# Optimization experiments

Measured on AMD Instinct MI355X. Metric: run time of the kernel, lower is better.

The kernel has to match this reference:

```python
import jax, jax.numpy as jnp
import numpy as np

LAMBDA_C = 10.0
LAMBDA_E = 10.0
LAMBDA_O = 10.0
H = 0.1          # proximity / thickness scale from __init__ h=0.1
EPS = 1e-8


def _pairwise_sq(a, b):
    # a [N,3], b [M,3] -> [N,M] squared distances
    return jnp.sum((a[:, None, :] - b[None, :, :]) ** 2, axis=-1)


def _total_loss(pred_vertices, face_probs, target_vertices, pred_faces, target_faces):
    pv, tv, probs = pred_vertices, target_vertices, face_probs

    # ---- chamfer loss (bidirectional mean of NN squared distances) ----
    d2_pt = _pairwise_sq(pv, tv)                       # [N, M]
    chamfer = d2_pt.min(axis=1).mean() + d2_pt.min(axis=0).mean()

    # ---- probabilistic surface distance via face barycenters ----
    tri = pv[pred_faces]                               # [F,3,3]
    ttri = tv[target_faces]                            # [Ft,3,3]
    bp = tri.mean(axis=1)                              # [F,3]
    bt = ttri.mean(axis=1)                             # [Ft,3]
    d2_f = _pairwise_sq(bp, bt)                        # [F,Ft]
    surface = (probs * d2_f.min(axis=1)).mean() + d2_f.min(axis=0).mean()

    # ---- shared pairwise geometry ----
    v0, v1, v2 = tri[:, 0], tri[:, 1], tri[:, 2]
    n = jnp.cross(v1 - v0, v2 - v0)                    # [F,3] face normals
    nhat = n / (jnp.linalg.norm(n, axis=-1, keepdims=True) + EPS)
    F_ = tri.shape[0]
    mask = 1.0 - jnp.eye(F_, dtype=pv.dtype)           # exclude self pairs
    cd2 = _pairwise_sq(bp, bp)                         # [F,F] centroid dist^2
    gate = jnp.exp(-cd2 / H)                           # soft spatial proximity gate

    # ---- triangle collision: vertices of tri j vs plane of tri i ----
    # s[i,j,v] = nhat_i . (tri[j,v] - v0_i)
    s = jnp.einsum('id,fvd->ifv', nhat, tri) - jnp.einsum('id,id->i', nhat, v0)[:, None, None]
    pen_col = jax.nn.relu(-(s.max(-1) * s.min(-1)))    # >0 iff tri j straddles plane i
    collision = (probs[:, None] * mask * gate * pen_col).sum() / F_

    # ---- edge crossing: segment-segment closest distance, all 9 edge pairs ----
    p = tri                                            # edge starts [F,3,3]
    q = jnp.roll(tri, -1, axis=1)                      # edge ends   [F,3,3]
    p1 = p[:, None, :, None, :]                        # [F,1,3,1,3]
    q1 = q[:, None, :, None, :]
    p2 = p[None, :, None, :, :]                        # [1,F,1,3,3]
    q2 = q[None, :, None, :, :]
    d1 = q1 - p1
    d2 = q2 - p2
    r = p1 - p2
    a = jnp.sum(d1 * d1, -1)
    e = jnp.sum(d2 * d2, -1)
    f = jnp.sum(d2 * r, -1)
    c = jnp.sum(d1 * r, -1)
    b = jnp.sum(d1 * d2, -1)
    denom = a * e - b * b
    sseg = jnp.clip((b * f - c * e) / (denom + EPS), 0.0, 1.0)
    tseg = jnp.clip((b * sseg + f) / (e + EPS), 0.0, 1.0)
    sseg = jnp.clip((b * tseg - c) / (a + EPS), 0.0, 1.0)
    cp1 = p1 + sseg[..., None] * d1
    cp2 = p2 + tseg[..., None] * d2
    dist = jnp.sqrt(jnp.sum((cp1 - cp2) ** 2, -1) + EPS)   # [F,F,3,3]
    pen_edge = jax.nn.relu(H - dist).sum((-1, -2))          # [F,F]
    edge_crossing = (probs[:, None] * mask * gate * pen_edge).sum() / F_

    # ---- triangle overlap: centroid of tri j close to plane of tri i ----
    dp = jnp.abs(jnp.einsum('id,jd->ij', nhat, bp) - jnp.einsum('id,id->i', nhat, v0)[:, None])
    pen_ov = jax.nn.relu(H - dp)                            # [F,F]
    overlap = (probs[:, None] * mask * gate * pen_ov).sum() / F_

    return (chamfer + surface
            + LAMBDA_C * collision
            + LAMBDA_E * edge_crossing
            + LAMBDA_O * overlap)


def setup_inputs() -> dict:
    key = jax.random.key(0)
    k1, k2, k3, k4, k5 = jax.random.split(key, 5)
    N, F, M, Ft = 512, 1024, 32768, 65536
    return {
        'pred_vertices': jax.random.normal(k1, (N, 3), dtype=jnp.float32),
        'face_probs': jax.random.uniform(k2, (F,), dtype=jnp.float32),
        'target_vertices': jax.random.normal(k3, (M, 3), dtype=jnp.float32),
        'pred_faces': jax.random.randint(k4, (F, 3), 0, N),
        'target_faces': jax.random.randint(k5, (Ft, 3), 0, M),
    }


def reference(pred_vertices, face_probs, target_vertices, pred_faces, target_faces):
    return _total_loss(pred_vertices, face_probs, target_vertices, pred_faces, target_faces)
```

## Files before the change

kernel.cpp:

```cpp
#include <hip/hip_runtime.h>
#include <hip/hip_bf16.h>
#include <math.h>

#define EPSF 1e-8f
#define HPARAM 0.1f
#define FB 16
#define NC 16
#define VB 8
#define NCM 16

__device__ __forceinline__ float waveReduceSum(float v) {
#pragma unroll
    for (int o = 32; o > 0; o >>= 1) v += __shfl_down(v, o, 64);
    return v;
}
__device__ __forceinline__ float waveReduceMin(float v) {
#pragma unroll
    for (int o = 32; o > 0; o >>= 1) v = fminf(v, __shfl_down(v, o, 64));
    return v;
}
__device__ __forceinline__ float blockSum(float s, float* red4) {
    s = waveReduceSum(s);
    int lane = threadIdx.x & 63, wid = threadIdx.x >> 6;
    if (lane == 0) red4[wid] = s;
    __syncthreads();
    return red4[0] + red4[1] + red4[2] + red4[3];
}
__device__ __forceinline__ float clamp01(float x) {
    return fminf(fmaxf(x, 0.0f), 1.0f);
}

__global__ __launch_bounds__(256) void k_pre(
    const float* __restrict__ pv, const int* __restrict__ pf,
    const float* __restrict__ tv, const int* __restrict__ tf,
    float* __restrict__ tri, float4* __restrict__ bp4,
    float* __restrict__ nhat, float* __restrict__ d0,
    float4* __restrict__ bt4, float4* __restrict__ tv4, float4* __restrict__ pv4,
    int N, int F, int M, int Ft)
{
    int nbF = (F + 255) >> 8, nbFt = (Ft + 255) >> 8, nbM = (M + 255) >> 8;
    int b = blockIdx.x, tid = threadIdx.x;
    if (b < nbF) {
        int i = b * 256 + tid;
        if (i >= F) return;
        int a = pf[i * 3 + 0], bb = pf[i * 3 + 1], c = pf[i * 3 + 2];
        float v0x = pv[a * 3], v0y = pv[a * 3 + 1], v0z = pv[a * 3 + 2];
        float v1x = pv[bb * 3], v1y = pv[bb * 3 + 1], v1z = pv[bb * 3 + 2];
        float v2x = pv[c * 3], v2y = pv[c * 3 + 1], v2z = pv[c * 3 + 2];
        tri[i * 9 + 0] = v0x; tri[i * 9 + 1] = v0y; tri[i * 9 + 2] = v0z;
        tri[i * 9 + 3] = v1x; tri[i * 9 + 4] = v1y; tri[i * 9 + 5] = v1z;
        tri[i * 9 + 6] = v2x; tri[i * 9 + 7] = v2y; tri[i * 9 + 8] = v2z;
        float bx = (v0x + v1x + v2x) / 3.0f;
        float by = (v0y + v1y + v2y) / 3.0f;
        float bz = (v0z + v1z + v2z) / 3.0f;
        bp4[i] = make_float4(bx, by, bz, bx * bx + by * by + bz * bz);
        float e1x = v1x - v0x, e1y = v1y - v0y, e1z = v1z - v0z;
        float e2x = v2x - v0x, e2y = v2y - v0y, e2z = v2z - v0z;
        float nx = e1y * e2z - e1z * e2y;
        float ny = e1z * e2x - e1x * e2z;
        float nz = e1x * e2y - e1y * e2x;
        float nrm = sqrtf(nx * nx + ny * ny + nz * nz);
        float inv = 1.0f / (nrm + EPSF);
        float hx = nx * inv, hy = ny * inv, hz = nz * inv;
        nhat[i * 3 + 0] = hx; nhat[i * 3 + 1] = hy; nhat[i * 3 + 2] = hz;
        d0[i] = hx * v0x + hy * v0y + hz * v0z;
    } else if (b < nbF + nbFt) {
        int j = (b - nbF) * 256 + tid;
        if (j >= Ft) return;
        int a = tf[j * 3 + 0], bb = tf[j * 3 + 1], c = tf[j * 3 + 2];
        float bx = (tv[a * 3 + 0] + tv[bb * 3 + 0] + tv[c * 3 + 0]) / 3.0f;
        float by = (tv[a * 3 + 1] + tv[bb * 3 + 1] + tv[c * 3 + 1]) / 3.0f;
        float bz = (tv[a * 3 + 2] + tv[bb * 3 + 2] + tv[c * 3 + 2]) / 3.0f;
        bt4[j] = make_float4(bx, by, bz, bx * bx + by * by + bz * bz);
    } else if (b < nbF + nbFt + nbM) {
        int j = (b - nbF - nbFt) * 256 + tid;
        if (j >= M) return;
        float x = tv[j * 3], y = tv[j * 3 + 1], z = tv[j * 3 + 2];
        tv4[j] = make_float4(x, y, z, x * x + y * y + z * z);
    } else {
        int j = (b - nbF - nbFt - nbM) * 256 + tid;
        if (j >= N) return;
        float x = pv[j * 3], y = pv[j * 3 + 1], z = pv[j * 3 + 2];
        pv4[j] = make_float4(x, y, z, x * x + y * y + z * z);
    }
}

__global__ __launch_bounds__(256) void k_mega(
    const float4* __restrict__ pv4, const float4* __restrict__ tv4,
    const float* __restrict__ tri, const float4* __restrict__ bp4,
    const float* __restrict__ nhat, const float* __restrict__ d0,
    const float* __restrict__ probs, const float4* __restrict__ bt4,
    float* __restrict__ chamAp, float* __restrict__ chamBp,
    float* __restrict__ surfAp, float* __restrict__ surfBp,
    float* __restrict__ pairp,
    int N, int F, int M, int Ft, int ncS, int ncC,
    int o1, int o2, int o3, int o4)
{
    __shared__ float4 sh4[1024];
    __shared__ float red4[4];
    int b = blockIdx.x;
    int tid = threadIdx.x;

    if (b < o1) {
        int fg = b & 63, chunk = b >> 6;
        int i0 = fg * FB;
        float m2x[FB], m2y[FB], m2z[FB], psq[FB], m[FB];
#pragma unroll
        for (int k = 0; k < FB; ++k) {
            float4 bb = bp4[i0 + k];
            m2x[k] = -2.0f * bb.x; m2y[k] = -2.0f * bb.y; m2z[k] = -2.0f * bb.z;
            psq[k] = bb.w;
            m[k] = 3.4e38f;
        }
        int TC = Ft / NC;
        int jend = chunk * TC + TC;
        for (int j = chunk * TC + tid; j < jend; j += 256) {
            float4 t = bt4[j];
#pragma unroll
            for (int k = 0; k < FB; ++k) {
                float acc = fmaf(m2x[k], t.x, fmaf(m2y[k], t.y, fmaf(m2z[k], t.z, psq[k] + t.w)));
                m[k] = fminf(m[k], acc);
            }
        }
        __shared__ float redA[4][FB];
#pragma unroll
        for (int k = 0; k < FB; ++k) m[k] = waveReduceMin(m[k]);
        int lane = tid & 63, wid = tid >> 6;
        if (lane == 0) {
#pragma unroll
            for (int k = 0; k < FB; ++k) redA[wid][k] = m[k];
        }
        __syncthreads();
        if (tid < FB) {
            float r = fminf(fminf(redA[0][tid], redA[1][tid]),
                            fminf(redA[2][tid], redA[3][tid]));
            surfAp[(i0 + tid) * NC + chunk] = r;
        }
    } else if (b < o2) {
        int rb = b - o1;
        int jg = rb & 63, c = rb >> 6;
        int CH = F / ncS;
        for (int t = tid; t < CH; t += 256) {
            float4 p = bp4[c * CH + t];
            sh4[t] = make_float4(-2.0f * p.x, -2.0f * p.y, -2.0f * p.z, p.w);
        }
        __syncthreads();
        int q = Ft >> 2;
        int j0 = jg * 256 + tid;
        float4 t0 = bt4[j0], t1 = bt4[j0 + q], t2 = bt4[j0 + 2 * q], t3 = bt4[j0 + 3 * q];
        float m0 = 3.4e38f, m1 = 3.4e38f, m2 = 3.4e38f, m3 = 3.4e38f;
#pragma unroll 4
        for (int i = 0; i < CH; ++i) {
            float4 p = sh4[i];
            m0 = fminf(m0, fmaf(p.x, t0.x, fmaf(p.y, t0.y, fmaf(p.z, t0.z, p.w + t0.w))));
            m1 = fminf(m1, fmaf(p.x, t1.x, fmaf(p.y, t1.y, fmaf(p.z, t1.z, p.w + t1.w))));
            m2 = fminf(m2, fmaf(p.x, t2.x, fmaf(p.y, t2.y, fmaf(p.z, t2.z, p.w + t2.w))));
            m3 = fminf(m3, fmaf(p.x, t3.x, fmaf(p.y, t3.y, fmaf(p.z, t3.z, p.w + t3.w))));
        }
        surfBp[c * Ft + j0] = m0;
        surfBp[c * Ft + j0 + q] = m1;
        surfBp[c * Ft + j0 + 2 * q] = m2;
        surfBp[c * Ft + j0 + 3 * q] = m3;
    } else if (b < o3) {
        int rb = b - o2;
        int vg = rb & 63, chunk = rb >> 6;
        int v0 = vg * VB;
        float m2x[VB], m2y[VB], m2z[VB], psq[VB], m[VB];
#pragma unroll
        for (int k = 0; k < VB; ++k) {
            float4 p = pv4[v0 + k];
            m2x[k] = -2.0f * p.x; m2y[k] = -2.0f * p.y; m2z[k] = -2.0f * p.z;
            psq[k] = p.w;
            m[k] = 3.4e38f;
        }
        int TC = M / NCM;
        int jend = chunk * TC + TC;
        for (int j = chunk * TC + tid; j < jend; j += 256) {
            float4 t = tv4[j];
#pragma unroll
            for (int k = 0; k < VB; ++k) {
                float acc = fmaf(m2x[k], t.x, fmaf(m2y[k], t.y, fmaf(m2z[k], t.z, psq[k] + t.w)));
                m[k] = fminf(m[k], acc);
            }
        }
        __shared__ float redC[4][VB];
#pragma unroll
        for (int k = 0; k < VB; ++k) m[k] = waveReduceMin(m[k]);
        int lane = tid & 63, wid = tid >> 6;
        if (lane == 0) {
#pragma unroll
            for (int k = 0; k < VB; ++k) redC[wid][k] = m[k];
        }
        __syncthreads();
        if (tid < VB) {
            float r = fminf(fminf(redC[0][tid], redC[1][tid]),
                            fminf(redC[2][tid], redC[3][tid]));
            chamAp[(v0 + tid) * NCM + chunk] = r;
        }
    } else if (b < o4) {
        int rb = b - o3;
        int jg = rb & 31, c = rb >> 5;
        int CH = N / ncC;
        for (int t = tid; t < CH; t += 256) {
            float4 p = pv4[c * CH + t];
            sh4[t] = make_float4(-2.0f * p.x, -2.0f * p.y, -2.0f * p.z, p.w);
        }
        __syncthreads();
        int q = M >> 2;
        int j0 = jg * 256 + tid;
        float4 t0 = tv4[j0], t1 = tv4[j0 + q], t2 = tv4[j0 + 2 * q], t3 = tv4[j0 + 3 * q];
        float m0 = 3.4e38f, m1 = 3.4e38f, m2 = 3.4e38f, m3 = 3.4e38f;
#pragma unroll 4
        for (int i = 0; i < CH; ++i) {
            float4 p = sh4[i];
            m0 = fminf(m0, fmaf(p.x, t0.x, fmaf(p.y, t0.y, fmaf(p.z, t0.z, p.w + t0.w))));
            m1 = fminf(m1, fmaf(p.x, t1.x, fmaf(p.y, t1.y, fmaf(p.z, t1.z, p.w + t1.w))));
            m2 = fminf(m2, fmaf(p.x, t2.x, fmaf(p.y, t2.y, fmaf(p.z, t2.z, p.w + t2.w))));
            m3 = fminf(m3, fmaf(p.x, t3.x, fmaf(p.y, t3.y, fmaf(p.z, t3.z, p.w + t3.w))));
        }
        chamBp[c * M + j0] = m0;
        chamBp[c * M + j0 + q] = m1;
        chamBp[c * M + j0 + 2 * q] = m2;
        chamBp[c * M + j0 + 3 * q] = m3;
    } else {
        int rb = b - o4;
        int bpF = F >> 8;
        int i = rb / bpF;
        int fg = rb % bpF;
        float* sTri = (float*)sh4;
        for (int t = tid; t < 256 * 9; t += 256) sTri[t] = tri[fg * 256 * 9 + t];
        __syncthreads();
        int f = fg * 256 + tid;

        float ti[9];
#pragma unroll
        for (int v = 0; v < 9; ++v) ti[v] = tri[i * 9 + v];
        float nix = nhat[i * 3], niy = nhat[i * 3 + 1], niz = nhat[i * 3 + 2];
        float di = d0[i];
        float4 bi = bp4[i];
        float pi = probs[i];

        float p1xa[3], p1ya[3], p1za[3], d1xa[3], d1ya[3], d1za[3], ava[3], rava[3];
#pragma unroll
        for (int e1 = 0; e1 < 3; ++e1) {
            int e1n = (e1 == 2) ? 0 : e1 + 1;
            p1xa[e1] = ti[e1 * 3]; p1ya[e1] = ti[e1 * 3 + 1]; p1za[e1] = ti[e1 * 3 + 2];
            d1xa[e1] = ti[e1n * 3] - p1xa[e1];
            d1ya[e1] = ti[e1n * 3 + 1] - p1ya[e1];
            d1za[e1] = ti[e1n * 3 + 2] - p1za[e1];
            ava[e1] = d1xa[e1] * d1xa[e1] + d1ya[e1] * d1ya[e1] + d1za[e1] * d1za[e1];
            rava[e1] = __builtin_amdgcn_rcpf(ava[e1] + EPSF);
        }

        float contrib = 0.0f;
        if (f != i) {
            float4 bf = bp4[f];
            float cdx = bi.x - bf.x, cdy = bi.y - bf.y, cdz = bi.z - bf.z;
            float cd2 = cdx * cdx + cdy * cdy + cdz * cdz;
            if (cd2 <= 2.0f) {
                float gate = __expf(-10.0f * cd2);
                float tf9[9];
#pragma unroll
                for (int v = 0; v < 9; ++v) tf9[v] = sTri[tid * 9 + v];
                float s0 = nix * tf9[0] + niy * tf9[1] + niz * tf9[2] - di;
                float s1 = nix * tf9[3] + niy * tf9[4] + niz * tf9[5] - di;
                float s2 = nix * tf9[6] + niy * tf9[7] + niz * tf9[8] - di;
                float smax = fmaxf(fmaxf(s0, s1), s2);
                float smin = fminf(fminf(s0, s1), s2);
                float pen_col = fmaxf(-(smax * smin), 0.0f);
                float dp = fabsf(nix * bf.x + niy * bf.y + niz * bf.z - di);
                float pen_ov = fmaxf(HPARAM - dp, 0.0f);
                float q2x[3], q2y[3], q2z[3], e2xa[3], e2ya[3], e2za[3], eva[3], reva[3];
#pragma unroll
                for (int e2 = 0; e2 < 3; ++e2) {
                    int e2n = (e2 == 2) ? 0 : e2 + 1;
                    q2x[e2] = tf9[e2 * 3]; q2y[e2] = tf9[e2 * 3 + 1]; q2z[e2] = tf9[e2 * 3 + 2];
                    e2xa[e2] = tf9[e2n * 3] - q2x[e2];
                    e2ya[e2] = tf9[e2n * 3 + 1] - q2y[e2];
                    e2za[e2] = tf9[e2n * 3 + 2] - q2z[e2];
                    eva[e2] = e2xa[e2] * e2xa[e2] + e2ya[e2] * e2ya[e2] + e2za[e2] * e2za[e2];
                    reva[e2] = __builtin_amdgcn_rcpf(eva[e2] + EPSF);
                }
                float pen_edge = 0.0f;
#pragma unroll
                for (int e1 = 0; e1 < 3; ++e1) {
#pragma unroll
                    for (int e2 = 0; e2 < 3; ++e2) {
                        float rx = p1xa[e1] - q2x[e2], ry = p1ya[e1] - q2y[e2], rz = p1za[e1] - q2z[e2];
                        float f_ = e2xa[e2] * rx + e2ya[e2] * ry + e2za[e2] * rz;
                        float c_ = d1xa[e1] * rx + d1ya[e1] * ry + d1za[e1] * rz;
                        float b_ = d1xa[e1] * e2xa[e2] + d1ya[e1] * e2ya[e2] + d1za[e1] * e2za[e2];
                        float denom = ava[e1] * eva[e2] - b_ * b_;
                        float rden = __builtin_amdgcn_rcpf(denom + EPSF);
                        float ss = clamp01(fmaf(-c_, eva[e2], b_ * f_) * rden);
                        float tt = clamp01(fmaf(b_, ss, f_) * reva[e2]);
                        ss = clamp01(fmaf(b_, tt, -c_) * rava[e1]);
                        float vx = fmaf(ss, d1xa[e1], p1xa[e1]) - fmaf(tt, e2xa[e2], q2x[e2]);
                        float vy = fmaf(ss, d1ya[e1], p1ya[e1]) - fmaf(tt, e2ya[e2], q2y[e2]);
                        float vz = fmaf(ss, d1za[e1], p1za[e1]) - fmaf(tt, e2za[e2], q2z[e2]);
                        float dist = __builtin_amdgcn_sqrtf(vx * vx + vy * vy + vz * vz + EPSF);
                        pen_edge += fmaxf(HPARAM - dist, 0.0f);
                    }
                }
                contrib = pi * gate * (pen_col + pen_ov + pen_edge);
            }
        }
        float s = blockSum(contrib, red4);
        if (tid == 0) pairp[rb] = s;
    }
}

__global__ __launch_bounds__(256) void k_reduce(
    const float* __restrict__ surfBp, int Ft, int ncS, float invFt,
    const float* __restrict__ chamBp, int M, int ncC, float invM,
    const float* __restrict__ chamAp, int N, float invN,
    const float* __restrict__ surfAp, const float* __restrict__ probs, int F, float invF,
    const float* __restrict__ pairp, float pairScale,
    float* __restrict__ smallp)
{
    __shared__ float red4[4];
    int b = blockIdx.x, tid = threadIdx.x;
    int nbS = Ft >> 8, nbC = M >> 8, nbA = N >> 8, nbSA = F >> 8;
    float s;
    if (b < nbS) {
        int j = b * 256 + tid;
        float r = 3.4e38f;
        for (int c = 0; c < ncS; ++c) r = fminf(r, surfBp[c * Ft + j]);
        s = r * invFt;
    } else if (b < nbS + nbC) {
        int j = (b - nbS) * 256 + tid;
        float r = 3.4e38f;
        for (int c = 0; c < ncC; ++c) r = fminf(r, chamBp[c * M + j]);
        s = r * invM;
    } else if (b < nbS + nbC + nbA) {
        int v = (b - nbS - nbC) * 256 + tid;
        float r = 3.4e38f;
#pragma unroll
        for (int c = 0; c < NCM; ++c) r = fminf(r, chamAp[v * NCM + c]);
        s = r * invN;
    } else if (b < nbS + nbC + nbA + nbSA) {
        int i = (b - nbS - nbC - nbA) * 256 + tid;
        float r = 3.4e38f;
#pragma unroll
        for (int c = 0; c < NC; ++c) r = fminf(r, surfAp[i * NC + c]);
        s = probs[i] * r * invF;
    } else {
        int t = (b - nbS - nbC - nbA - nbSA) * 256 + tid;
        s = pairp[t] * pairScale;
    }
    float r = blockSum(s, red4);
    if (tid == 0) smallp[b] = r;
}

__global__ __launch_bounds__(256) void k_fin(
    const float* __restrict__ smallp, int n, float* __restrict__ out)
{
    __shared__ float red4[4];
    float s = 0.0f;
    for (int t = threadIdx.x; t < n; t += 256) s += smallp[t];
    float r = blockSum(s, red4);
    if (threadIdx.x == 0) out[0] = r;
}

extern "C" void kernel_launch(void* const* d_in, const int* in_sizes, int n_in,
                              void* d_out, int out_size, void* d_ws, size_t ws_size,
                              hipStream_t stream) {
    const float* pv    = (const float*)d_in[0];
    const float* probs = (const float*)d_in[1];
    const float* tv    = (const float*)d_in[2];
    const int*   pf    = (const int*)d_in[3];
    const int*   tf    = (const int*)d_in[4];
    float* out = (float*)d_out;

    int N  = in_sizes[0] / 3;
    int F  = in_sizes[1];
    int M  = in_sizes[2] / 3;
    int Ft = in_sizes[4] / 3;

    int nP = F * (F / 256);

    size_t baseFloats = (size_t)F * 13 + (size_t)F * 4 + (size_t)Ft * 4
                      + (size_t)M * 4 + (size_t)N * 4
                      + (size_t)N * NCM + (size_t)F * NC + (size_t)nP + 512;
    int ncS = 8, ncC = 8;
    if (ws_size < (baseFloats + (size_t)8 * Ft + (size_t)8 * M) * 4) {
        ncS = 2; ncC = 2;
        if (ws_size < (baseFloats + (size_t)2 * Ft + (size_t)2 * M) * 4) { ncS = 1; ncC = 1; }
    }

    float* ws = (float*)d_ws;
    float* w_tri    = ws;
    float* w_nhat   = w_tri + F * 9;
    float* w_d0     = w_nhat + F * 3;
    float4* w_bp4   = (float4*)(w_d0 + F);
    float4* w_bt4   = w_bp4 + F;
    float4* w_tv4   = w_bt4 + Ft;
    float4* w_pv4   = w_tv4 + M;
    float* w_chamAp = (float*)(w_pv4 + N);
    float* w_surfAp = w_chamAp + N * NCM;
    float* w_pair   = w_surfAp + F * NC;
    float* w_small  = w_pair + nP;
    float* w_surfBp = w_small + 512;
    float* w_chamBp = w_surfBp + (size_t)ncS * Ft;

    int gSurfA = (F / FB) * NC;
    int gSurfB = (Ft / 4 / 256) * ncS;
    int gChamA = (N / VB) * NCM;
    int gChamB = (M / 4 / 256) * ncC;
    int o1 = gSurfA;
    int o2 = o1 + gSurfB;
    int o3 = o2 + gChamA;
    int o4 = o3 + gChamB;
    int gTot = o4 + nP;

    int nSmall = (Ft >> 8) + (M >> 8) + (N >> 8) + (F >> 8) + (nP >> 8);
    int gPre = (F + 255) / 256 + (Ft + 255) / 256 + (M + 255) / 256 + (N + 255) / 256;

    k_pre<<<gPre, 256, 0, stream>>>(
        pv, pf, tv, tf, w_tri, w_bp4, w_nhat, w_d0, w_bt4, w_tv4, w_pv4, N, F, M, Ft);
    k_mega<<<gTot, 256, 0, stream>>>(
        w_pv4, w_tv4, w_tri, w_bp4, w_nhat, w_d0, probs, w_bt4,
        w_chamAp, w_chamBp, w_surfAp, w_surfBp, w_pair,
        N, F, M, Ft, ncS, ncC, o1, o2, o3, o4);
    k_reduce<<<nSmall, 256, 0, stream>>>(
        w_surfBp, Ft, ncS, 1.0f / (float)Ft,
        w_chamBp, M, ncC, 1.0f / (float)M,
        w_chamAp, N, 1.0f / (float)N,
        w_surfAp, probs, F, 1.0f / (float)F,
        w_pair, 10.0f / (float)F,
        w_small);
    k_fin<<<1, 256, 0, stream>>>(w_small, nSmall, out);
}
```

Measured before the change: 50.60 us.

## Fuse column-min passes into row-min loops and compact pair candidates

The separate column-direction nearest-neighbour passes for surface and chamfer are removed. Instead, the row-min loops also write a per-group column minimum for each target point, which k_reduce then folds across groups. This reuses the distance evaluations already computed instead of recomputing the full distance matrix twice. It costs far more partial writes (64 groups per target for both surface and chamfer) and a heavier reduction pass. The pair kernel also compacts proximity-passing candidates with ballot and prefix sums to cut divergence, and skips the nine square roots when the minimum edge distance exceeds H.

```diff
diff --git a/kernel.cpp b/kernel.cpp
--- a/kernel.cpp
+++ b/kernel.cpp
@@ -93,10 +93,9 @@
     float* __restrict__ chamAp, float* __restrict__ chamBp,
     float* __restrict__ surfAp, float* __restrict__ surfBp,
     float* __restrict__ pairp,
-    int N, int F, int M, int Ft, int ncS, int ncC,
-    int o1, int o2, int o3, int o4)
+    int N, int F, int M, int Ft,
+    int o1, int o2)
 {
-    __shared__ float4 sh4[1024];
     __shared__ float red4[4];
     int b = blockIdx.x;
     int tid = threadIdx.x;
@@ -116,11 +115,14 @@
         int jend = chunk * TC + TC;
         for (int j = chunk * TC + tid; j < jend; j += 256) {
             float4 t = bt4[j];
+            float jm = 3.4e38f;
 #pragma unroll
             for (int k = 0; k < FB; ++k) {
                 float acc = fmaf(m2x[k], t.x, fmaf(m2y[k], t.y, fmaf(m2z[k], t.z, psq[k] + t.w)));
                 m[k] = fminf(m[k], acc);
-            }
+                jm = fminf(jm, acc);
+            }
+            surfBp[fg * Ft + j] = jm;
         }
         __shared__ float redA[4][FB];
 #pragma unroll
@@ -138,31 +140,6 @@
         }
     } else if (b < o2) {
         int rb = b - o1;
-        int jg = rb & 63, c = rb >> 6;
-        int CH = F / ncS;
-        for (int t = tid; t < CH; t += 256) {
-            float4 p = bp4[c * CH + t];
-            sh4[t] = make_float4(-2.0f * p.x, -2.0f * p.y, -2.0f * p.z, p.w);
-        }
-        __syncthreads();
-        int q = Ft >> 2;
-        int j0 = jg * 256 + tid;
-        float4 t0 = bt4[j0], t1 = bt4[j0 + q], t2 = bt4[j0 + 2 * q], t3 = bt4[j0 + 3 * q];
-        float m0 = 3.4e38f, m1 = 3.4e38f, m2 = 3.4e38f, m3 = 3.4e38f;
-#pragma unroll 4
-        for (int i = 0; i < CH; ++i) {
-            float4 p = sh4[i];
-            m0 = fminf(m0, fmaf(p.x, t0.x, fmaf(p.y, t0.y, fmaf(p.z, t0.z, p.w + t0.w))));
-            m1 = fminf(m1, fmaf(p.x, t1.x, fmaf(p.y, t1.y, fmaf(p.z, t1.z, p.w + t1.w))));
-            m2 = fminf(m2, fmaf(p.x, t2.x, fmaf(p.y, t2.y, fmaf(p.z, t2.z, p.w + t2.w))));
-            m3 = fminf(m3, fmaf(p.x, t3.x, fmaf(p.y, t3.y, fmaf(p.z, t3.z, p.w + t3.w))));
-        }
-        surfBp[c * Ft + j0] = m0;
-        surfBp[c * Ft + j0 + q] = m1;
-        surfBp[c * Ft + j0 + 2 * q] = m2;
-        surfBp[c * Ft + j0 + 3 * q] = m3;
-    } else if (b < o3) {
-        int rb = b - o2;
         int vg = rb & 63, chunk = rb >> 6;
         int v0 = vg * VB;
         float m2x[VB], m2y[VB], m2z[VB], psq[VB], m[VB];
@@ -177,11 +154,14 @@
         int jend = chunk * TC + TC;
         for (int j = chunk * TC + tid; j < jend; j += 256) {
             float4 t = tv4[j];
+            float jm = 3.4e38f;
 #pragma unroll
             for (int k = 0; k < VB; ++k) {
                 float acc = fmaf(m2x[k], t.x, fmaf(m2y[k], t.y, fmaf(m2z[k], t.z, psq[k] + t.w)));
                 m[k] = fminf(m[k], acc);
-            }
+                jm = fminf(jm, acc);
+            }
+            chamBp[vg * M + j] = jm;
         }
         __shared__ float redC[4][VB];
 #pragma unroll
@@ -197,40 +177,16 @@
                             fminf(redC[2][tid], redC[3][tid]));
             chamAp[(v0 + tid) * NCM + chunk] = r;
         }
-    } else if (b < o4) {
-        int rb = b - o3;
-        int jg = rb & 31, c = rb >> 5;
-        int CH = N / ncC;
-        for (int t = tid; t < CH; t += 256) {
-            float4 p = pv4[c * CH + t];
-            sh4[t] = make_float4(-2.0f * p.x, -2.0f * p.y, -2.0f * p.z, p.w);
-        }
-        __syncthreads();
-        int q = M >> 2;
-        int j0 = jg * 256 + tid;
-        float4 t0 = tv4[j0], t1 = tv4[j0 + q], t2 = tv4[j0 + 2 * q], t3 = tv4[j0 + 3 * q];
-        float m0 = 3.4e38f, m1 = 3.4e38f, m2 = 3.4e38f, m3 = 3.4e38f;
-#pragma unroll 4
-        for (int i = 0; i < CH; ++i) {
-            float4 p = sh4[i];
-            m0 = fminf(m0, fmaf(p.x, t0.x, fmaf(p.y, t0.y, fmaf(p.z, t0.z, p.w + t0.w))));
-            m1 = fminf(m1, fmaf(p.x, t1.x, fmaf(p.y, t1.y, fmaf(p.z, t1.z, p.w + t1.w))));
-            m2 = fminf(m2, fmaf(p.x, t2.x, fmaf(p.y, t2.y, fmaf(p.z, t2.z, p.w + t2.w))));
-            m3 = fminf(m3, fmaf(p.x, t3.x, fmaf(p.y, t3.y, fmaf(p.z, t3.z, p.w + t3.w))));
-        }
-        chamBp[c * M + j0] = m0;
-        chamBp[c * M + j0 + q] = m1;
-        chamBp[c * M + j0 + 2 * q] = m2;
-        chamBp[c * M + j0 + 3 * q] = m3;
     } else {
-        int rb = b - o4;
+        __shared__ float sTri[256 * 9];
+        __shared__ int slist[256];
+        __shared__ float scd2[256];
+        __shared__ int scnt[4];
+        int rb = b - o2;
         int bpF = F >> 8;
         int i = rb / bpF;
         int fg = rb % bpF;
-        float* sTri = (float*)sh4;
         for (int t = tid; t < 256 * 9; t += 256) sTri[t] = tri[fg * 256 * 9 + t];
-        __syncthreads();
-        int f = fg * 256 + tid;
 
         float ti[9];
 #pragma unroll
@@ -252,58 +208,81 @@
             rava[e1] = __builtin_amdgcn_rcpf(ava[e1] + EPSF);
         }
 
+        int f = fg * 256 + tid;
+        float4 bft = bp4[f];
+        float cdx = bi.x - bft.x, cdy = bi.y - bft.y, cdz = bi.z - bft.z;
+        float cd2 = cdx * cdx + cdy * cdy + cdz * cdz;
+        bool pass = (f != i) && (cd2 <= 2.0f);
+        unsigned long long mask = __ballot(pass);
+        int lane = tid & 63, wid = tid >> 6;
+        if (lane == 0) scnt[wid] = __popcll(mask);
+        __syncthreads();
+        int base = 0;
+#pragma unroll
+        for (int w = 0; w < 4; ++w) base += (w < wid) ? scnt[w] : 0;
+        int nCand = scnt[0] + scnt[1] + scnt[2] + scnt[3];
+        int pfx = __popcll(mask & ((1ULL << lane) - 1ULL));
+        if (pass) { slist[base + pfx] = tid; scd2[base + pfx] = cd2; }
+        __syncthreads();
+
         float contrib = 0.0f;
-        if (f != i) {
-            float4 bf = bp4[f];
-            float cdx = bi.x - bf.x, cdy = bi.y - bf.y, cdz = bi.z - bf.z;
-            float cd2 = cdx * cdx + cdy * cdy + cdz * cdz;
-            if (cd2 <= 2.0f) {
-                float gate = __expf(-10.0f * cd2);
-                float tf9[9];
-#pragma unroll
-                for (int v = 0; v < 9; ++v) tf9[v] = sTri[tid * 9 + v];
-                float s0 = nix * tf9[0] + niy * tf9[1] + niz * tf9[2] - di;
-                float s1 = nix * tf9[3] + niy * tf9[4] + niz * tf9[5] - di;
-                float s2 = nix * tf9[6] + niy * tf9[7] + niz * tf9[8] - di;
-                float smax = fmaxf(fmaxf(s0, s1), s2);
-                float smin = fminf(fminf(s0, s1), s2);
-                float pen_col = fmaxf(-(smax * smin), 0.0f);
-                float dp = fabsf(nix * bf.x + niy * bf.y + niz * bf.z - di);
-                float pen_ov = fmaxf(HPARAM - dp, 0.0f);
-                float q2x[3], q2y[3], q2z[3], e2xa[3], e2ya[3], e2za[3], eva[3], reva[3];
+        if (tid < nCand) {
+            int src = slist[tid];
+            float cc = scd2[tid];
+            float gate = __expf(-10.0f * cc);
+            float4 bf = bp4[fg * 256 + src];
+            float tf9[9];
+#pragma unroll
+            for (int v = 0; v < 9; ++v) tf9[v] = sTri[src * 9 + v];
+            float s0 = nix * tf9[0] + niy * tf9[1] + niz * tf9[2] - di;
+            float s1 = nix * tf9[3] + niy * tf9[4] + niz * tf9[5] - di;
+            float s2 = nix * tf9[6] + niy * tf9[7] + niz * tf9[8] - di;
+            float smax = fmaxf(fmaxf(s0, s1), s2);
+            float smin = fminf(fminf(s0, s1), s2);
+            float pen_col = fmaxf(-(smax * smin), 0.0f);
+            float dp = fabsf(nix * bf.x + niy * bf.y + niz * bf.z - di);
+            float pen_ov = fmaxf(HPARAM - dp, 0.0f);
+            float q2x[3], q2y[3], q2z[3], e2xa[3], e2ya[3], e2za[3], eva[3], reva[3];
+#pragma unroll
+            for (int e2 = 0; e2 < 3; ++e2) {
+                int e2n = (e2 == 2) ? 0 : e2 + 1;
+                q2x[e2] = tf9[e2 * 3]; q2y[e2] = tf9[e2 * 3 + 1]; q2z[e2] = tf9[e2 * 3 + 2];
+                e2xa[e2] = tf9[e2n * 3] - q2x[e2];
+                e2ya[e2] = tf9[e2n * 3 + 1] - q2y[e2];
+                e2za[e2] = tf9[e2n * 3 + 2] - q2z[e2];
+                eva[e2] = e2xa[e2] * e2xa[e2] + e2ya[e2] * e2ya[e2] + e2za[e2] * e2za[e2];
+                reva[e2] = __builtin_amdgcn_rcpf(eva[e2] + EPSF);
+            }
+            float d2v[9];
+            float dminv = 3.4e38f;
+#pragma unroll
+            for (int e1 = 0; e1 < 3; ++e1) {
 #pragma unroll
                 for (int e2 = 0; e2 < 3; ++e2) {
-                    int e2n = (e2 == 2) ? 0 : e2 + 1;
-                    q2x[e2] = tf9[e2 * 3]; q2y[e2] = tf9[e2 * 3 + 1]; q2z[e2] = tf9[e2 * 3 + 2];
-                    e2xa[e2] = tf9[e2n * 3] - q2x[e2];
-                    e2ya[e2] = tf9[e2n * 3 + 1] - q2y[e2];
-                    e2za[e2] = tf9[e2n * 3 + 2] - q2z[e2];
-                    eva[e2] = e2xa[e2] * e2xa[e2] + e2ya[e2] * e2ya[e2] + e2za[e2] * e2za[e2];
-                    reva[e2] = __builtin_amdgcn_rcpf(eva[e2] + EPSF);
+                    float rx = p1xa[e1] - q2x[e2], ry = p1ya[e1] - q2y[e2], rz = p1za[e1] - q2z[e2];
+                    float f_ = e2xa[e2] * rx + e2ya[e2] * ry + e2za[e2] * rz;
+                    float c_ = d1xa[e1] * rx + d1ya[e1] * ry + d1za[e1] * rz;
+                    float b_ = d1xa[e1] * e2xa[e2] + d1ya[e1] * e2ya[e2] + d1za[e1] * e2za[e2];
+                    float denom = ava[e1] * eva[e2] - b_ * b_;
+                    float rden = __builtin_amdgcn_rcpf(denom + EPSF);
+                    float ss = clamp01(fmaf(-c_, eva[e2], b_ * f_) * rden);
+                    float tt = clamp01(fmaf(b_, ss, f_) * reva[e2]);
+                    ss = clamp01(fmaf(b_, tt, -c_) * rava[e1]);
+                    float vx = fmaf(ss, d1xa[e1], p1xa[e1]) - fmaf(tt, e2xa[e2], q2x[e2]);
+                    float vy = fmaf(ss, d1ya[e1], p1ya[e1]) - fmaf(tt, e2ya[e2], q2y[e2]);
+                    float vz = fmaf(ss, d1za[e1], p1za[e1]) - fmaf(tt, e2za[e2], q2z[e2]);
+                    float dd = vx * vx + vy * vy + vz * vz;
+                    d2v[e1 * 3 + e2] = dd;
+                    dminv = fminf(dminv, dd);
                 }
-                float pen_edge = 0.0f;
-#pragma unroll
-                for (int e1 = 0; e1 < 3; ++e1) {
-#pragma unroll
-                    for (int e2 = 0; e2 < 3; ++e2) {
-                        float rx = p1xa[e1] - q2x[e2], ry = p1ya[e1] - q2y[e2], rz = p1za[e1] - q2z[e2];
-                        float f_ = e2xa[e2] * rx + e2ya[e2] * ry + e2za[e2] * rz;
-                        float c_ = d1xa[e1] * rx + d1ya[e1] * ry + d1za[e1] * rz;
-                        float b_ = d1xa[e1] * e2xa[e2] + d1ya[e1] * e2ya[e2] + d1za[e1] * e2za[e2];
-                        float denom = ava[e1] * eva[e2] - b_ * b_;
-                        float rden = __builtin_amdgcn_rcpf(denom + EPSF);
-                        float ss = clamp01(fmaf(-c_, eva[e2], b_ * f_) * rden);
-                        float tt = clamp01(fmaf(b_, ss, f_) * reva[e2]);
-                        ss = clamp01(fmaf(b_, tt, -c_) * rava[e1]);
-                        float vx = fmaf(ss, d1xa[e1], p1xa[e1]) - fmaf(tt, e2xa[e2], q2x[e2]);
-                        float vy = fmaf(ss, d1ya[e1], p1ya[e1]) - fmaf(tt, e2ya[e2], q2y[e2]);
-                        float vz = fmaf(ss, d1za[e1], p1za[e1]) - fmaf(tt, e2za[e2], q2z[e2]);
-                        float dist = __builtin_amdgcn_sqrtf(vx * vx + vy * vy + vz * vz + EPSF);
-                        pen_edge += fmaxf(HPARAM - dist, 0.0f);
-                    }
-                }
-                contrib = pi * gate * (pen_col + pen_ov + pen_edge);
-            }
+            }
+            float pen_edge = 0.0f;
+            if (dminv + EPSF < HPARAM * HPARAM) {
+#pragma unroll
+                for (int q = 0; q < 9; ++q)
+                    pen_edge += fmaxf(HPARAM - __builtin_amdgcn_sqrtf(d2v[q] + EPSF), 0.0f);
+            }
+            contrib = pi * gate * (pen_col + pen_ov + pen_edge);
         }
         float s = blockSum(contrib, red4);
         if (tid == 0) pairp[rb] = s;
@@ -311,8 +290,8 @@
 }
 
 __global__ __launch_bounds__(256) void k_reduce(
-    const float* __restrict__ surfBp, int Ft, int ncS, float invFt,
-    const float* __restrict__ chamBp, int M, int ncC, float invM,
+    const float* __restrict__ surfBp, int Ft, int nGS, float invFt,
+    const float* __restrict__ chamBp, int M, int nGC, float invM,
     const float* __restrict__ chamAp, int N, float invN,
     const float* __restrict__ surfAp, const float* __restrict__ probs, int F, float invF,
     const float* __restrict__ pairp, float pairScale,
@@ -325,12 +304,12 @@
     if (b < nbS) {
         int j = b * 256 + tid;
         float r = 3.4e38f;
-        for (int c = 0; c < ncS; ++c) r = fminf(r, surfBp[c * Ft + j]);
+        for (int c = 0; c < nGS; ++c) r = fminf(r, surfBp[c * Ft + j]);
         s = r * invFt;
     } else if (b < nbS + nbC) {
         int j = (b - nbS) * 256 + tid;
         float r = 3.4e38f;
-        for (int c = 0; c < ncC; ++c) r = fminf(r, chamBp[c * M + j]);
+        for (int c = 0; c < nGC; ++c) r = fminf(r, chamBp[c * M + j]);
         s = r * invM;
     } else if (b < nbS + nbC + nbA) {
         int v = (b - nbS - nbC) * 256 + tid;
@@ -377,16 +356,9 @@
     int M  = in_sizes[2] / 3;
     int Ft = in_sizes[4] / 3;
 
-    int nP = F * (F / 256);
-
-    size_t baseFloats = (size_t)F * 13 + (size_t)F * 4 + (size_t)Ft * 4
-                      + (size_t)M * 4 + (size_t)N * 4
-                      + (size_t)N * NCM + (size_t)F * NC + (size_t)nP + 512;
-    int ncS = 8, ncC = 8;
-    if (ws_size < (baseFloats + (size_t)8 * Ft + (size_t)8 * M) * 4) {
-        ncS = 2; ncC = 2;
-        if (ws_size < (baseFloats + (size_t)2 * Ft + (size_t)2 * M) * 4) { ncS = 1; ncC = 1; }
-    }
+    int nP  = F * (F / 256);
+    int nGS = F / FB;
+    int nGC = N / VB;
 
     float* ws = (float*)d_ws;
     float* w_tri    = ws;
@@ -401,17 +373,11 @@
     float* w_pair   = w_surfAp + F * NC;
     float* w_small  = w_pair + nP;
     float* w_surfBp = w_small + 512;
-    float* w_chamBp = w_surfBp + (size_t)ncS * Ft;
-
-    int gSurfA = (F / FB) * NC;
-    int gSurfB = (Ft / 4 / 256) * ncS;
-    int gChamA = (N / VB) * NCM;
-    int gChamB = (M / 4 / 256) * ncC;
-    int o1 = gSurfA;
-    int o2 = o1 + gSurfB;
-    int o3 = o2 + gChamA;
-    int o4 = o3 + gChamB;
-    int gTot = o4 + nP;
+    float* w_chamBp = w_surfBp + (size_t)nGS * Ft;
+
+    int o1 = (F / FB) * NC;
+    int o2 = o1 + (N / VB) * NCM;
+    int gTot = o2 + nP;
 
     int nSmall = (Ft >> 8) + (M >> 8) + (N >> 8) + (F >> 8) + (nP >> 8);
     int gPre = (F + 255) / 256 + (Ft + 255) / 256 + (M + 255) / 256 + (N + 255) / 256;
@@ -421,10 +387,10 @@
     k_mega<<<gTot, 256, 0, stream>>>(
         w_pv4, w_tv4, w_tri, w_bp4, w_nhat, w_d0, probs, w_bt4,
         w_chamAp, w_chamBp, w_surfAp, w_surfBp, w_pair,
-        N, F, M, Ft, ncS, ncC, o1, o2, o3, o4);
+        N, F, M, Ft, o1, o2);
     k_reduce<<<nSmall, 256, 0, stream>>>(
-        w_surfBp, Ft, ncS, 1.0f / (float)Ft,
-        w_chamBp, M, ncC, 1.0f / (float)M,
+        w_surfBp, Ft, nGS, 1.0f / (float)Ft,
+        w_chamBp, M, nGC, 1.0f / (float)M,
         w_chamAp, N, 1.0f / (float)N,
         w_surfAp, probs, F, 1.0f / (float)F,
         w_pair, 10.0f / (float)F,
```

Result: slower. 65.63 us (+29.7%).

## Compact gated pair candidates per block, hoist norm terms, fuse final reduce

Applied to the files above, without the earlier changes.

The pairwise penalty section now handles several faces per block. It compacts the candidate pairs that pass the proximity gate into a shared list using ballot and prefix counts, so the active lanes run the heavy segment math densely instead of diverging. The per-pair edge sqrt work is skipped unless the minimum squared distance is inside the threshold. The squared-norm terms in the nearest-neighbour min loops are moved out of the inner loop and added after the min. The final single-block kernel is replaced by a last-block-done atomic counter inside the reduce kernel, which adds extra __syncthreads per face iteration and a counter reset.

```diff
diff --git a/kernel.cpp b/kernel.cpp
--- a/kernel.cpp
+++ b/kernel.cpp
@@ -8,6 +8,7 @@
 #define NC 16
 #define VB 8
 #define NCM 16
+#define TI 4
 
 __device__ __forceinline__ float waveReduceSum(float v) {
 #pragma unroll
@@ -36,8 +37,10 @@
     float* __restrict__ tri, float4* __restrict__ bp4,
     float* __restrict__ nhat, float* __restrict__ d0,
     float4* __restrict__ bt4, float4* __restrict__ tv4, float4* __restrict__ pv4,
+    int* __restrict__ cnt,
     int N, int F, int M, int Ft)
 {
+    if (blockIdx.x == 0 && threadIdx.x == 0) *cnt = 0;
     int nbF = (F + 255) >> 8, nbFt = (Ft + 255) >> 8, nbM = (M + 255) >> 8;
     int b = blockIdx.x, tid = threadIdx.x;
     if (b < nbF) {
@@ -94,7 +97,7 @@
     float* __restrict__ surfAp, float* __restrict__ surfBp,
     float* __restrict__ pairp,
     int N, int F, int M, int Ft, int ncS, int ncC,
-    int o1, int o2, int o3, int o4)
+    int o1, int o2, int o3)
 {
     __shared__ float4 sh4[1024];
     __shared__ float red4[4];
@@ -104,12 +107,11 @@
     if (b < o1) {
         int fg = b & 63, chunk = b >> 6;
         int i0 = fg * FB;
-        float m2x[FB], m2y[FB], m2z[FB], psq[FB], m[FB];
+        float m2x[FB], m2y[FB], m2z[FB], m[FB];
 #pragma unroll
         for (int k = 0; k < FB; ++k) {
             float4 bb = bp4[i0 + k];
             m2x[k] = -2.0f * bb.x; m2y[k] = -2.0f * bb.y; m2z[k] = -2.0f * bb.z;
-            psq[k] = bb.w;
             m[k] = 3.4e38f;
         }
         int TC = Ft / NC;
@@ -118,7 +120,7 @@
             float4 t = bt4[j];
 #pragma unroll
             for (int k = 0; k < FB; ++k) {
-                float acc = fmaf(m2x[k], t.x, fmaf(m2y[k], t.y, fmaf(m2z[k], t.z, psq[k] + t.w)));
+                float acc = fmaf(m2x[k], t.x, fmaf(m2y[k], t.y, fmaf(m2z[k], t.z, t.w)));
                 m[k] = fminf(m[k], acc);
             }
         }
@@ -134,7 +136,7 @@
         if (tid < FB) {
             float r = fminf(fminf(redA[0][tid], redA[1][tid]),
                             fminf(redA[2][tid], redA[3][tid]));
-            surfAp[(i0 + tid) * NC + chunk] = r;
+            surfAp[(i0 + tid) * NC + chunk] = r + bp4[i0 + tid].w;
         }
     } else if (b < o2) {
         int rb = b - o1;
@@ -152,25 +154,24 @@
 #pragma unroll 4
         for (int i = 0; i < CH; ++i) {
             float4 p = sh4[i];
-            m0 = fminf(m0, fmaf(p.x, t0.x, fmaf(p.y, t0.y, fmaf(p.z, t0.z, p.w + t0.w))));
-            m1 = fminf(m1, fmaf(p.x, t1.x, fmaf(p.y, t1.y, fmaf(p.z, t1.z, p.w + t1.w))));
-            m2 = fminf(m2, fmaf(p.x, t2.x, fmaf(p.y, t2.y, fmaf(p.z, t2.z, p.w + t2.w))));
-            m3 = fminf(m3, fmaf(p.x, t3.x, fmaf(p.y, t3.y, fmaf(p.z, t3.z, p.w + t3.w))));
-        }
-        surfBp[c * Ft + j0] = m0;
-        surfBp[c * Ft + j0 + q] = m1;
-        surfBp[c * Ft + j0 + 2 * q] = m2;
-        surfBp[c * Ft + j0 + 3 * q] = m3;
+            m0 = fminf(m0, fmaf(p.x, t0.x, fmaf(p.y, t0.y, fmaf(p.z, t0.z, p.w))));
+            m1 = fminf(m1, fmaf(p.x, t1.x, fmaf(p.y, t1.y, fmaf(p.z, t1.z, p.w))));
+            m2 = fminf(m2, fmaf(p.x, t2.x, fmaf(p.y, t2.y, fmaf(p.z, t2.z, p.w))));
+            m3 = fminf(m3, fmaf(p.x, t3.x, fmaf(p.y, t3.y, fmaf(p.z, t3.z, p.w))));
+        }
+        surfBp[c * Ft + j0] = m0 + t0.w;
+        surfBp[c * Ft + j0 + q] = m1 + t1.w;
+        surfBp[c * Ft + j0 + 2 * q] = m2 + t2.w;
+        surfBp[c * Ft + j0 + 3 * q] = m3 + t3.w;
     } else if (b < o3) {
         int rb = b - o2;
         int vg = rb & 63, chunk = rb >> 6;
         int v0 = vg * VB;
-        float m2x[VB], m2y[VB], m2z[VB], psq[VB], m[VB];
+        float m2x[VB], m2y[VB], m2z[VB], m[VB];
 #pragma unroll
         for (int k = 0; k < VB; ++k) {
             float4 p = pv4[v0 + k];
             m2x[k] = -2.0f * p.x; m2y[k] = -2.0f * p.y; m2z[k] = -2.0f * p.z;
-            psq[k] = p.w;
             m[k] = 3.4e38f;
         }
         int TC = M / NCM;
@@ -179,7 +180,7 @@
             float4 t = tv4[j];
 #pragma unroll
             for (int k = 0; k < VB; ++k) {
-                float acc = fmaf(m2x[k], t.x, fmaf(m2y[k], t.y, fmaf(m2z[k], t.z, psq[k] + t.w)));
+                float acc = fmaf(m2x[k], t.x, fmaf(m2y[k], t.y, fmaf(m2z[k], t.z, t.w)));
                 m[k] = fminf(m[k], acc);
             }
         }
@@ -195,9 +196,9 @@
         if (tid < VB) {
             float r = fminf(fminf(redC[0][tid], redC[1][tid]),
                             fminf(redC[2][tid], redC[3][tid]));
-            chamAp[(v0 + tid) * NCM + chunk] = r;
-        }
-    } else if (b < o4) {
+            chamAp[(v0 + tid) * NCM + chunk] = r + pv4[v0 + tid].w;
+        }
+    } else if (b < o3 + (M >> 10) * ncC) {
         int rb = b - o3;
         int jg = rb & 31, c = rb >> 5;
         int CH = N / ncC;
@@ -213,55 +214,73 @@
 #pragma unroll 4
         for (int i = 0; i < CH; ++i) {
             float4 p = sh4[i];
-            m0 = fminf(m0, fmaf(p.x, t0.x, fmaf(p.y, t0.y, fmaf(p.z, t0.z, p.w + t0.w))));
-            m1 = fminf(m1, fmaf(p.x, t1.x, fmaf(p.y, t1.y, fmaf(p.z, t1.z, p.w + t1.w))));
-            m2 = fminf(m2, fmaf(p.x, t2.x, fmaf(p.y, t2.y, fmaf(p.z, t2.z, p.w + t2.w))));
-            m3 = fminf(m3, fmaf(p.x, t3.x, fmaf(p.y, t3.y, fmaf(p.z, t3.z, p.w + t3.w))));
-        }
-        chamBp[c * M + j0] = m0;
-        chamBp[c * M + j0 + q] = m1;
-        chamBp[c * M + j0 + 2 * q] = m2;
-        chamBp[c * M + j0 + 3 * q] = m3;
+            m0 = fminf(m0, fmaf(p.x, t0.x, fmaf(p.y, t0.y, fmaf(p.z, t0.z, p.w))));
+            m1 = fminf(m1, fmaf(p.x, t1.x, fmaf(p.y, t1.y, fmaf(p.z, t1.z, p.w))));
+            m2 = fminf(m2, fmaf(p.x, t2.x, fmaf(p.y, t2.y, fmaf(p.z, t2.z, p.w))));
+            m3 = fminf(m3, fmaf(p.x, t3.x, fmaf(p.y, t3.y, fmaf(p.z, t3.z, p.w))));
+        }
+        chamBp[c * M + j0] = m0 + t0.w;
+        chamBp[c * M + j0 + q] = m1 + t1.w;
+        chamBp[c * M + j0 + 2 * q] = m2 + t2.w;
+        chamBp[c * M + j0 + 3 * q] = m3 + t3.w;
     } else {
-        int rb = b - o4;
+        __shared__ int slist[256];
+        __shared__ float scd2[256];
+        __shared__ int scnt[4];
+        int rb = b - (o3 + (M >> 10) * ncC);
         int bpF = F >> 8;
-        int i = rb / bpF;
+        int ig = rb / bpF;
         int fg = rb % bpF;
         float* sTri = (float*)sh4;
         for (int t = tid; t < 256 * 9; t += 256) sTri[t] = tri[fg * 256 * 9 + t];
         __syncthreads();
-        int f = fg * 256 + tid;
-
-        float ti[9];
-#pragma unroll
-        for (int v = 0; v < 9; ++v) ti[v] = tri[i * 9 + v];
-        float nix = nhat[i * 3], niy = nhat[i * 3 + 1], niz = nhat[i * 3 + 2];
-        float di = d0[i];
-        float4 bi = bp4[i];
-        float pi = probs[i];
-
-        float p1xa[3], p1ya[3], p1za[3], d1xa[3], d1ya[3], d1za[3], ava[3], rava[3];
-#pragma unroll
-        for (int e1 = 0; e1 < 3; ++e1) {
-            int e1n = (e1 == 2) ? 0 : e1 + 1;
-            p1xa[e1] = ti[e1 * 3]; p1ya[e1] = ti[e1 * 3 + 1]; p1za[e1] = ti[e1 * 3 + 2];
-            d1xa[e1] = ti[e1n * 3] - p1xa[e1];
-            d1ya[e1] = ti[e1n * 3 + 1] - p1ya[e1];
-            d1za[e1] = ti[e1n * 3 + 2] - p1za[e1];
-            ava[e1] = d1xa[e1] * d1xa[e1] + d1ya[e1] * d1ya[e1] + d1za[e1] * d1za[e1];
-            rava[e1] = __builtin_amdgcn_rcpf(ava[e1] + EPSF);
-        }
-
+
+        int lane = tid & 63, wid = tid >> 6;
         float contrib = 0.0f;
-        if (f != i) {
-            float4 bf = bp4[f];
-            float cdx = bi.x - bf.x, cdy = bi.y - bf.y, cdz = bi.z - bf.z;
+#pragma unroll 1
+        for (int ii = 0; ii < TI; ++ii) {
+            int i = ig * TI + ii;
+            float ti[9];
+#pragma unroll
+            for (int v = 0; v < 9; ++v) ti[v] = tri[i * 9 + v];
+            float nix = nhat[i * 3], niy = nhat[i * 3 + 1], niz = nhat[i * 3 + 2];
+            float di = d0[i];
+            float4 bi = bp4[i];
+            float pi = probs[i];
+            float p1xa[3], p1ya[3], p1za[3], d1xa[3], d1ya[3], d1za[3], ava[3], rava[3];
+#pragma unroll
+            for (int e1 = 0; e1 < 3; ++e1) {
+                int e1n = (e1 == 2) ? 0 : e1 + 1;
+                p1xa[e1] = ti[e1 * 3]; p1ya[e1] = ti[e1 * 3 + 1]; p1za[e1] = ti[e1 * 3 + 2];
+                d1xa[e1] = ti[e1n * 3] - p1xa[e1];
+                d1ya[e1] = ti[e1n * 3 + 1] - p1ya[e1];
+                d1za[e1] = ti[e1n * 3 + 2] - p1za[e1];
+                ava[e1] = d1xa[e1] * d1xa[e1] + d1ya[e1] * d1ya[e1] + d1za[e1] * d1za[e1];
+                rava[e1] = __builtin_amdgcn_rcpf(ava[e1] + EPSF);
+            }
+            int f = fg * 256 + tid;
+            float4 bft = bp4[f];
+            float cdx = bi.x - bft.x, cdy = bi.y - bft.y, cdz = bi.z - bft.z;
             float cd2 = cdx * cdx + cdy * cdy + cdz * cdz;
-            if (cd2 <= 2.0f) {
-                float gate = __expf(-10.0f * cd2);
+            bool pass = (f != i) && (cd2 <= 2.0f);
+            unsigned long long mask = __ballot(pass);
+            if (lane == 0) scnt[wid] = __popcll(mask);
+            __syncthreads();
+            int base = 0;
+#pragma unroll
+            for (int w = 0; w < 4; ++w) base += (w < wid) ? scnt[w] : 0;
+            int nCand = scnt[0] + scnt[1] + scnt[2] + scnt[3];
+            int pfx = __popcll(mask & ((1ULL << lane) - 1ULL));
+            if (pass) { slist[base + pfx] = tid; scd2[base + pfx] = cd2; }
+            __syncthreads();
+
+            if (tid < nCand) {
+                int src = slist[tid];
+                float gate = __expf(-10.0f * scd2[tid]);
+                float4 bf = bp4[fg * 256 + src];
                 float tf9[9];
 #pragma unroll
-                for (int v = 0; v < 9; ++v) tf9[v] = sTri[tid * 9 + v];
+                for (int v = 0; v < 9; ++v) tf9[v] = sTri[src * 9 + v];
                 float s0 = nix * tf9[0] + niy * tf9[1] + niz * tf9[2] - di;
                 float s1 = nix * tf9[3] + niy * tf9[4] + niz * tf9[5] - di;
                 float s2 = nix * tf9[6] + niy * tf9[7] + niz * tf9[8] - di;
@@ -281,7 +300,8 @@
                     eva[e2] = e2xa[e2] * e2xa[e2] + e2ya[e2] * e2ya[e2] + e2za[e2] * e2za[e2];
                     reva[e2] = __builtin_amdgcn_rcpf(eva[e2] + EPSF);
                 }
-                float pen_edge = 0.0f;
+                float d2v[9];
+                float dminv = 3.4e38f;
 #pragma unroll
                 for (int e1 = 0; e1 < 3; ++e1) {
 #pragma unroll
@@ -298,12 +318,20 @@
                         float vx = fmaf(ss, d1xa[e1], p1xa[e1]) - fmaf(tt, e2xa[e2], q2x[e2]);
                         float vy = fmaf(ss, d1ya[e1], p1ya[e1]) - fmaf(tt, e2ya[e2], q2y[e2]);
                         float vz = fmaf(ss, d1za[e1], p1za[e1]) - fmaf(tt, e2za[e2], q2z[e2]);
-                        float dist = __builtin_amdgcn_sqrtf(vx * vx + vy * vy + vz * vz + EPSF);
-                        pen_edge += fmaxf(HPARAM - dist, 0.0f);
+                        float dd = vx * vx + vy * vy + vz * vz;
+                        d2v[e1 * 3 + e2] = dd;
+                        dminv = fminf(dminv, dd);
                     }
                 }
-                contrib = pi * gate * (pen_col + pen_ov + pen_edge);
+                float pen_edge = 0.0f;
+                if (dminv + EPSF < HPARAM * HPARAM) {
+#pragma unroll
+                    for (int qq = 0; qq < 9; ++qq)
+                        pen_edge += fmaxf(HPARAM - __builtin_amdgcn_sqrtf(d2v[qq] + EPSF), 0.0f);
+                }
+                contrib += pi * gate * (pen_col + pen_ov + pen_edge);
             }
+            __syncthreads();
         }
         float s = blockSum(contrib, red4);
         if (tid == 0) pairp[rb] = s;
@@ -315,10 +343,12 @@
     const float* __restrict__ chamBp, int M, int ncC, float invM,
     const float* __restrict__ chamAp, int N, float invN,
     const float* __restrict__ surfAp, const float* __restrict__ probs, int F, float invF,
-    const float* __restrict__ pairp, float pairScale,
-    float* __restrict__ smallp)
+    const float* __restrict__ pairp, int nPB, float pairScale,
+    float* __restrict__ smallp, int nb, int* __restrict__ cnt,
+    float* __restrict__ out)
 {
     __shared__ float red4[4];
+    __shared__ int isLast;
     int b = blockIdx.x, tid = threadIdx.x;
     int nbS = Ft >> 8, nbC = M >> 8, nbA = N >> 8, nbSA = F >> 8;
     float s;
@@ -346,20 +376,22 @@
         s = probs[i] * r * invF;
     } else {
         int t = (b - nbS - nbC - nbA - nbSA) * 256 + tid;
-        s = pairp[t] * pairScale;
+        s = (t < nPB) ? pairp[t] * pairScale : 0.0f;
     }
     float r = blockSum(s, red4);
     if (tid == 0) smallp[b] = r;
-}
-
-__global__ __launch_bounds__(256) void k_fin(
-    const float* __restrict__ smallp, int n, float* __restrict__ out)
-{
-    __shared__ float red4[4];
-    float s = 0.0f;
-    for (int t = threadIdx.x; t < n; t += 256) s += smallp[t];
-    float r = blockSum(s, red4);
-    if (threadIdx.x == 0) out[0] = r;
+    if (tid == 0) {
+        __threadfence();
+        isLast = (atomicAdd(cnt, 1) == nb - 1) ? 1 : 0;
+    }
+    __syncthreads();
+    if (isLast) {
+        __threadfence();
+        float s2 = 0.0f;
+        for (int t = tid; t < nb; t += 256) s2 += smallp[t];
+        float r2 = blockSum(s2, red4);
+        if (tid == 0) { out[0] = r2; *cnt = 0; }
+    }
 }
 
 extern "C" void kernel_launch(void* const* d_in, const int* in_sizes, int n_in,
@@ -377,11 +409,12 @@
     int M  = in_sizes[2] / 3;
     int Ft = in_sizes[4] / 3;
 
-    int nP = F * (F / 256);
+    int bpF = F >> 8;
+    int nPB = (F / TI) * bpF;
 
     size_t baseFloats = (size_t)F * 13 + (size_t)F * 4 + (size_t)Ft * 4
                       + (size_t)M * 4 + (size_t)N * 4
-                      + (size_t)N * NCM + (size_t)F * NC + (size_t)nP + 512;
+                      + (size_t)N * NCM + (size_t)F * NC + (size_t)nPB + 512 + 16;
     int ncS = 8, ncC = 8;
     if (ws_size < (baseFloats + (size_t)8 * Ft + (size_t)8 * M) * 4) {
         ncS = 2; ncC = 2;
@@ -399,35 +432,32 @@
     float* w_chamAp = (float*)(w_pv4 + N);
     float* w_surfAp = w_chamAp + N * NCM;
     float* w_pair   = w_surfAp + F * NC;
-    float* w_small  = w_pair + nP;
-    float* w_surfBp = w_small + 512;
+    float* w_small  = w_pair + nPB;
+    int*   w_cnt    = (int*)(w_small + 512);
+    float* w_surfBp = w_small + 512 + 4;
     float* w_chamBp = w_surfBp + (size_t)ncS * Ft;
 
-    int gSurfA = (F / FB) * NC;
-    int gSurfB = (Ft / 4 / 256) * ncS;
-    int gChamA = (N / VB) * NCM;
+    int o1 = (F / FB) * NC;
+    int o2 = o1 + (Ft / 4 / 256) * ncS;
+    int o3 = o2 + (N / VB) * NCM;
     int gChamB = (M / 4 / 256) * ncC;
-    int o1 = gSurfA;
-    int o2 = o1 + gSurfB;
-    int o3 = o2 + gChamA;
-    int o4 = o3 + gChamB;
-    int gTot = o4 + nP;
-
-    int nSmall = (Ft >> 8) + (M >> 8) + (N >> 8) + (F >> 8) + (nP >> 8);
+    int gTot = o3 + gChamB + nPB;
+
+    int nSmall = (Ft >> 8) + (M >> 8) + (N >> 8) + (F >> 8) + ((nPB + 255) >> 8);
     int gPre = (F + 255) / 256 + (Ft + 255) / 256 + (M + 255) / 256 + (N + 255) / 256;
 
     k_pre<<<gPre, 256, 0, stream>>>(
-        pv, pf, tv, tf, w_tri, w_bp4, w_nhat, w_d0, w_bt4, w_tv4, w_pv4, N, F, M, Ft);
+        pv, pf, tv, tf, w_tri, w_bp4, w_nhat, w_d0, w_bt4, w_tv4, w_pv4, w_cnt,
+        N, F, M, Ft);
     k_mega<<<gTot, 256, 0, stream>>>(
         w_pv4, w_tv4, w_tri, w_bp4, w_nhat, w_d0, probs, w_bt4,
         w_chamAp, w_chamBp, w_surfAp, w_surfBp, w_pair,
-        N, F, M, Ft, ncS, ncC, o1, o2, o3, o4);
+        N, F, M, Ft, ncS, ncC, o1, o2, o3);
     k_reduce<<<nSmall, 256, 0, stream>>>(
         w_surfBp, Ft, ncS, 1.0f / (float)Ft,
         w_chamBp, M, ncC, 1.0f / (float)M,
         w_chamAp, N, 1.0f / (float)N,
         w_surfAp, probs, F, 1.0f / (float)F,
-        w_pair, 10.0f / (float)F,
-        w_small);
-    k_fin<<<1, 256, 0, stream>>>(w_small, nSmall, out);
-}
+        w_pair, nPB, 10.0f / (float)F,
+        w_small, nSmall, w_cnt, out);
+}
```

Result: slower. 59.94 us (+18.5%).
